# Kernel tuning notes

Measured on AMD Instinct MI355X. Metric: run time of the kernel, lower is better.

Reference implementation:

```python
import jax, jax.numpy as jnp
import numpy as np

WS = 8          # window_size
NH = 8          # num_heads
DIM = 512
INNER = 512
CDIM = 128
CINNER = 128
SHIFTED = True
EPS = 1e-6
N = WS * WS     # tokens per window
SCALE = 1.0 / np.sqrt(INNER // NH + CINNER // NH)  # SDPA scale over fused (feat+coord) head dim


def _rmsnorm(x, g):
    return x * jax.lax.rsqrt(jnp.mean(x * x, axis=-1, keepdims=True) + EPS) * g


def _rel_indices():
    idx = np.array([[x, y] for x in range(WS) for y in range(WS)])
    ri = idx[None, :, :] - idx[:, None, :] + WS - 1
    return ri[..., 0], ri[..., 1]


def _shift_mask(Wh, Ww):
    s = WS
    k = s * (s // 2)
    row = np.zeros((N, N), np.float32)
    row[-k:, :-k] = -np.inf
    row[:-k, -k:] = -np.inf
    col = row.reshape(s, s, s, s).transpose(1, 0, 3, 2).reshape(N, N)
    m = np.zeros((Wh, Ww, N, N), np.float32)
    m[:, -1] += row
    m[-1, :] += col
    return jnp.asarray(m)


def setup_inputs() -> dict:
    key = jax.random.key(0)
    ks = jax.random.split(key, 16)
    B, h, w = 4, 128, 128

    def lin(k, fan_in, fan_out):
        return jax.random.normal(k, (fan_in, fan_out), jnp.float32) * (fan_in ** -0.5)

    return {
        "features": jax.random.normal(ks[0], (B, h, w, DIM), jnp.float32),
        "coords": jax.random.normal(ks[1], (B, h, w, CDIM), jnp.float32),
        "w_fqk": lin(ks[2], DIM, 2 * INNER),
        "b_fqk": jnp.zeros((2 * INNER,), jnp.float32),
        "g_fqk": jnp.ones((2 * INNER,), jnp.float32),
        "w_cqk": lin(ks[3], CDIM, 2 * CINNER),
        "b_cqk": jnp.zeros((2 * CINNER,), jnp.float32),
        "g_cqk": jnp.ones((2 * CINNER,), jnp.float32),
        "w_v": lin(ks[4], DIM, INNER),
        "b_v": jnp.zeros((INNER,), jnp.float32),
        "w_out": lin(ks[5], INNER, DIM),
        "b_out": jnp.zeros((DIM,), jnp.float32),
        "pos_emb": jax.random.normal(ks[6], (2 * WS - 1, 2 * WS - 1), jnp.float32),
    }


def reference(features, coords, w_fqk, b_fqk, g_fqk, w_cqk, b_cqk, g_cqk,
              w_v, b_v, w_out, b_out, pos_emb):
    B, h, w, _ = features.shape
    pad_h = (WS - h % WS) % WS
    pad_w = (WS - w % WS) % WS
    H_pad, W_pad = h + pad_h, w + pad_w
    Wh, Ww = H_pad // WS, W_pad // WS

    fqk = _rmsnorm(features @ w_fqk + b_fqk, g_fqk)
    f_q, f_k = jnp.split(fqk, 2, axis=-1)
    cqk = _rmsnorm(coords @ w_cqk + b_cqk, g_cqk)
    c_q, c_k = jnp.split(cqk, 2, axis=-1)
    f_v = features @ w_v + b_v

    def win(t):
        t = jnp.pad(t, ((0, 0), (0, pad_h), (0, pad_w), (0, 0)))
        if SHIFTED:
            t = jnp.roll(t, (-(WS // 2), -(WS // 2)), axis=(1, 2))
        D = t.shape[-1]
        t = t.reshape(B, Wh, WS, Ww, WS, D).transpose(0, 1, 3, 2, 4, 5)
        return t.reshape(B, Wh, Ww, N, D)

    def heads(t):
        D = t.shape[-1]
        return t.reshape(B, Wh, Ww, N, NH, D // NH)

    fq, fk, fv = heads(win(f_q)), heads(win(f_k)), heads(win(f_v))
    cq, ck = heads(win(c_q)), heads(win(c_k))

    # fused feature + coordinate QK scores, per head per window
    scores = (jnp.einsum('bxyqhd,bxykhd->bxyhqk', fq, fk)
              + jnp.einsum('bxyqhd,bxykhd->bxyhqk', cq, ck)) * SCALE

    ri0, ri1 = _rel_indices()
    pos_bias = pos_emb[ri0, ri1]  # (N, N)
    bias = pos_bias[None, None, None, None]
    if SHIFTED:
        bias = bias + _shift_mask(Wh, Ww)[None, :, :, None]
    scores = scores + bias

    attn = jax.nn.softmax(scores, axis=-1)
    out = jnp.einsum('bxyhqk,bxykhd->bxyqhd', attn, fv)
    out = out.reshape(B, Wh, Ww, N, INNER)

    # un-window
    out = out.reshape(B, Wh, Ww, WS, WS, INNER).transpose(0, 1, 3, 2, 4, 5)
    out = out.reshape(B, H_pad, W_pad, INNER)
    if SHIFTED:
        out = jnp.roll(out, (WS // 2, WS // 2), axis=(1, 2))
    out = out[:, :h, :w, :]
    return out @ w_out + b_out
```

## Files before the change

### kernel.cpp

```cpp
#include <hip/hip_runtime.h>
#include <hip/hip_bf16.h>
#include <type_traits>

using bf16 = __hip_bfloat16;
typedef __bf16 bf16x8 __attribute__((ext_vector_type(8)));
typedef float f32x4 __attribute__((ext_vector_type(4)));

static constexpr int TOKENS = 4 * 128 * 128;
#define SCALE_F 0.11180339887498949f
#define EPS_F 1e-6f

__device__ __forceinline__ float u2f(unsigned short u) {
  union { unsigned int i; float f; } c; c.i = (unsigned int)u << 16; return c.f;
}
__device__ __forceinline__ unsigned short f2u(float f) {
  bf16 h = __float2bfloat16(f); return *reinterpret_cast<unsigned short*>(&h);
}
__device__ __forceinline__ float b2f(bf16 v) { return __bfloat162float(v); }
__device__ __forceinline__ int4 cvt8(const float* p) {
  float4 a = ((const float4*)p)[0], b = ((const float4*)p)[1];
  union { int4 i4; unsigned short s[8]; } u;
  u.s[0] = f2u(a.x); u.s[1] = f2u(a.y); u.s[2] = f2u(a.z); u.s[3] = f2u(a.w);
  u.s[4] = f2u(b.x); u.s[5] = f2u(b.y); u.s[6] = f2u(b.z); u.s[7] = f2u(b.w);
  return u.i4;
}
__device__ __forceinline__ void gload16(const bf16* g, bf16* l) {
  __builtin_amdgcn_global_load_lds(
      (const __attribute__((address_space(1))) unsigned int*)g,
      (__attribute__((address_space(3))) unsigned int*)l, 16, 0, 0);
}

__global__ void convert_k(const float* __restrict__ in, bf16* __restrict__ out,
                          long n) {
  long i = ((long)blockIdx.x * 256 + threadIdx.x) * 8;
  long stride = (long)gridDim.x * 256 * 8;
  for (; i < n; i += stride) *(int4*)(out + i) = cvt8(in + i);
}

__global__ void transpose_k(const float* __restrict__ in, bf16* __restrict__ out,
                            int K, int N) {
  int i = blockIdx.x * 256 + threadIdx.x;
  if (i >= K * N) return;
  int k = i / N, n = i - k * N;
  out[(size_t)n * K + k] = __float2bfloat16(in[i]);
}

__global__ void biascat_k(const float* __restrict__ a, const float* __restrict__ b,
                          float* __restrict__ o) {
  int i = blockIdx.x * 256 + threadIdx.x;
  if (i < 1536) o[i] = i < 1024 ? a[i] : b[i - 1024];
}

template <typename TC, int SSNX>
__global__ __launch_bounds__(256) void gemm128_k(
    const bf16* __restrict__ A, const bf16* __restrict__ Wt,
    const float* __restrict__ bias, TC* __restrict__ C,
    float* __restrict__ ssq, int M, int N, int K) {
  __shared__ __align__(16) bf16 sA[2][4096];
  __shared__ __align__(16) bf16 sB[2][4096];
  const int t = threadIdx.x, lane = t & 63, wave = t >> 6;
  const int wr = wave >> 1, wc = wave & 1;
  const int nwg = gridDim.x * gridDim.y;
  int id = blockIdx.y * gridDim.x + blockIdx.x;
  if ((nwg & 7) == 0) id = (id & 7) * (nwg >> 3) + (id >> 3);
  const int bx = id % gridDim.x, by = id / gridDim.x;
  const int bm = by * 128, bn = bx * 128;
  const int l15 = lane & 15, kg = lane >> 4;
  f32x4 acc[4][4] = {};

  const int srow = t >> 2;
  const int ske = ((t & 3) ^ ((srow >> 1) & 3)) * 8;
  const bf16* pA0 = A + (size_t)(bm + srow) * K + ske;
  const bf16* pA1 = A + (size_t)(bm + 64 + srow) * K + ske;
  const bf16* pB0 = Wt + (size_t)(bn + srow) * K + ske;
  const bf16* pB1 = Wt + (size_t)(bn + 64 + srow) * K + ske;
  const int wo = wave * 512;

  gload16(pA0, &sA[0][wo]);
  gload16(pA1, &sA[0][2048 + wo]);
  gload16(pB0, &sB[0][wo]);
  gload16(pB1, &sB[0][2048 + wo]);
  __syncthreads();

  const int nt = K >> 5;
  int cur = 0;
  for (int tt = 0; tt < nt; ++tt) {
    if (tt + 1 < nt) {
      pA0 += 32; pA1 += 32; pB0 += 32; pB1 += 32;
      gload16(pA0, &sA[cur ^ 1][wo]);
      gload16(pA1, &sA[cur ^ 1][2048 + wo]);
      gload16(pB0, &sB[cur ^ 1][wo]);
      gload16(pB1, &sB[cur ^ 1][2048 + wo]);
    }
    bf16x8 wf[4], xf[4];
#pragma unroll
    for (int i = 0; i < 4; ++i) {
      int frow = wc * 64 + i * 16 + l15;
      int xrow = wr * 64 + i * 16 + l15;
      wf[i] = *(const bf16x8*)(&sB[cur][frow * 32 + ((kg ^ ((frow >> 1) & 3)) * 8)]);
      xf[i] = *(const bf16x8*)(&sA[cur][xrow * 32 + ((kg ^ ((xrow >> 1) & 3)) * 8)]);
    }
#pragma unroll
    for (int i = 0; i < 4; ++i)
#pragma unroll
      for (int j = 0; j < 4; ++j)
        acc[i][j] = __builtin_amdgcn_mfma_f32_16x16x32_bf16(wf[i], xf[j], acc[i][j], 0, 0, 0);
    __syncthreads();
    cur ^= 1;
  }

  float bvi[4][4];
#pragma unroll
  for (int i = 0; i < 4; ++i) {
    float4 b4 = *(const float4*)(bias + bn + wc * 64 + i * 16 + kg * 4);
    bvi[i][0] = b4.x; bvi[i][1] = b4.y; bvi[i][2] = b4.z; bvi[i][3] = b4.w;
  }
#pragma unroll
  for (int j = 0; j < 4; ++j) {
    const int token = bm + wr * 64 + j * 16 + l15;
    float ssum = 0.f;
#pragma unroll
    for (int i = 0; i < 4; ++i) {
      float v0 = acc[i][j][0] + bvi[i][0];
      float v1 = acc[i][j][1] + bvi[i][1];
      float v2 = acc[i][j][2] + bvi[i][2];
      float v3 = acc[i][j][3] + bvi[i][3];
      const size_t off = (size_t)token * N + bn + wc * 64 + i * 16 + kg * 4;
      if constexpr (std::is_same<TC, float>::value) {
        *(float4*)(C + off) = float4{v0, v1, v2, v3};
      } else {
        ushort4 pk{f2u(v0), f2u(v1), f2u(v2), f2u(v3)};
        *(ushort4*)(C + off) = pk;
      }
      if constexpr (SSNX > 0)
        ssum += v0 * v0 + v1 * v1 + v2 * v2 + v3 * v3;
    }
    if constexpr (SSNX > 0) {
      ssum += __shfl_xor(ssum, 16);
      ssum += __shfl_xor(ssum, 32);
      if (bx < SSNX && kg == 0)
        ssq[(size_t)token * (SSNX * 2) + bx * 2 + wc] = ssum;
    }
  }
}

__global__ void finalize_rs_k(const float* __restrict__ pf,
                              const float* __restrict__ pc,
                              float* __restrict__ rsf, float* __restrict__ rsc) {
  int i = blockIdx.x * 256 + threadIdx.x;
  if (i >= TOKENS) return;
  float s = 0.f;
#pragma unroll
  for (int j = 0; j < 16; ++j) s += pf[(size_t)i * 16 + j];
  rsf[i] = rsqrtf(s * (1.f / 1024.f) + EPS_F);
  float c = 0.f;
#pragma unroll
  for (int j = 0; j < 4; ++j) c += pc[(size_t)i * 4 + j];
  rsc[i] = rsqrtf(c * (1.f / 256.f) + EPS_F);
}

__global__ __launch_bounds__(256) void attn_mfma_k(
    const bf16* __restrict__ qkv, const bf16* __restrict__ cqk,
    const float* __restrict__ pos, const float* __restrict__ g_fqk,
    const float* __restrict__ g_cqk, const float* __restrict__ rs_f,
    const float* __restrict__ rs_c, bf16* __restrict__ aout) {
  __shared__ __align__(16) bf16 sQ[64][104], sK[64][104];
  __shared__ __align__(16) bf16 sVt[64][72];
  __shared__ __align__(16) bf16 sP[64][72];
  __shared__ float sPos[15][15];
  __shared__ float sRsF[64], sRsC[64];
  const int t = threadIdx.x, lane = t & 63, wave = t >> 6;
  const int head = blockIdx.x & 7;
  const int wid = blockIdx.x >> 3;
  const int wx = wid & 15, wy = (wid >> 4) & 15, b = wid >> 8;

  for (int i = t; i < 225; i += 256) sPos[i / 15][i % 15] = pos[i];
  if (t < 64) {
    const int y = ((wy << 3) + (t >> 3) + 4) & 127;
    const int x = ((wx << 3) + (t & 7) + 4) & 127;
    const size_t tok = ((size_t)b << 14) | (y << 7) | x;
    sRsF[t] = rs_f[tok];
    sRsC[t] = rs_c[tok];
  }
  {
    const int n = t >> 2, p = t & 3;
    const int y = ((wy << 3) + (n >> 3) + 4) & 127;
    const int x = ((wx << 3) + (n & 7) + 4) & 127;
    const size_t tok = ((size_t)b << 14) | (y << 7) | x;
    const bf16* row = qkv + tok * 1536;
    const int4* qp = (const int4*)(row + head * 64 + p * 16);
    ((int4*)&sQ[n][p * 16])[0] = qp[0];
    ((int4*)&sQ[n][p * 16])[1] = qp[1];
    {
      const bf16* kpp = row + 512 + head * 64 + p * 16;
      const float* gq = g_fqk + head * 64 + p * 16;
      const float* gk = g_fqk + 512 + head * 64 + p * 16;
      union { int4 v[2]; unsigned short s[16]; } kt;
#pragma unroll
      for (int i = 0; i < 16; ++i)
        kt.s[i] = f2u(b2f(kpp[i]) * gq[i] * gk[i]);
      ((int4*)&sK[n][p * 16])[0] = kt.v[0];
      ((int4*)&sK[n][p * 16])[1] = kt.v[1];
    }
    const bf16* vp = row + 1024 + head * 64 + p * 16;
#pragma unroll
    for (int i = 0; i < 16; ++i) sVt[p * 16 + i][n] = vp[i];
    const bf16* crow = cqk + tok * 256;
    if (p == 0) {
      const int4* cp = (const int4*)(crow + head * 16);
      ((int4*)&sQ[n][64])[0] = cp[0];
      ((int4*)&sQ[n][64])[1] = cp[1];
    } else if (p == 1) {
      const bf16* ckp = crow + 128 + head * 16;
      const float* gcq = g_cqk + head * 16;
      const float* gck = g_cqk + 128 + head * 16;
      union { int4 v[2]; unsigned short s[16]; } ct;
#pragma unroll
      for (int i = 0; i < 16; ++i)
        ct.s[i] = f2u(b2f(ckp[i]) * gcq[i] * gck[i]);
      ((int4*)&sK[n][64])[0] = ct.v[0];
      ((int4*)&sK[n][64])[1] = ct.v[1];
    } else if (p == 2) {
      ((int4*)&sQ[n][80])[0] = int4{0, 0, 0, 0};
      ((int4*)&sQ[n][80])[1] = int4{0, 0, 0, 0};
    } else {
      ((int4*)&sK[n][80])[0] = int4{0, 0, 0, 0};
      ((int4*)&sK[n][80])[1] = int4{0, 0, 0, 0};
    }
  }
  __syncthreads();

  const int l15 = lane & 15, kg = lane >> 4;
  bf16x8 qa[3];
#pragma unroll
  for (int ko = 0; ko < 3; ++ko)
    qa[ko] = *(const bf16x8*)&sQ[wave * 16 + l15][ko * 32 + kg * 8];
  f32x4 saccf[4] = {}, saccc[4] = {};
#pragma unroll
  for (int j = 0; j < 4; ++j) {
#pragma unroll
    for (int ko = 0; ko < 2; ++ko) {
      bf16x8 kb = *(const bf16x8*)&sK[j * 16 + l15][ko * 32 + kg * 8];
      saccf[j] = __builtin_amdgcn_mfma_f32_16x16x32_bf16(qa[ko], kb, saccf[j], 0, 0, 0);
    }
    bf16x8 kb2 = *(const bf16x8*)&sK[j * 16 + l15][64 + kg * 8];
    saccc[j] = __builtin_amdgcn_mfma_f32_16x16x32_bf16(qa[2], kb2, saccc[j], 0, 0, 0);
  }

  const bool lastx = (wx == 15), lasty = (wy == 15);
  float rqf[4], rqc[4];
#pragma unroll
  for (int r = 0; r < 4; ++r) {
    rqf[r] = sRsF[wave * 16 + kg * 4 + r];
    rqc[r] = sRsC[wave * 16 + kg * 4 + r];
  }
  float sv[4][4], mx[4], sum[4], inv[4];
#pragma unroll
  for (int r = 0; r < 4; ++r) mx[r] = -1e30f;
#pragma unroll
  for (int j = 0; j < 4; ++j) {
    int kcol = j * 16 + l15, kh = kcol >> 3, kw = kcol & 7;
    float rkf = sRsF[kcol], rkc = sRsC[kcol];
#pragma unroll
    for (int r = 0; r < 4; ++r) {
      int q = wave * 16 + kg * 4 + r, qh = q >> 3, qw = q & 7;
      bool msk = (lastx && ((qh >= 4) != (kh >= 4))) ||
                 (lasty && ((qw >= 4) != (kw >= 4)));
      float raw = saccf[j][r] * rqf[r] * rkf + saccc[j][r] * rqc[r] * rkc;
      float val = msk ? -1e30f : raw * SCALE_F + sPos[kh - qh + 7][kw - qw + 7];
      sv[j][r] = val;
      mx[r] = fmaxf(mx[r], val);
    }
  }
#pragma unroll
  for (int m = 1; m < 16; m <<= 1)
#pragma unroll
    for (int r = 0; r < 4; ++r) mx[r] = fmaxf(mx[r], __shfl_xor(mx[r], m));
#pragma unroll
  for (int r = 0; r < 4; ++r) sum[r] = 0.f;
#pragma unroll
  for (int j = 0; j < 4; ++j) {
    int kcol = j * 16 + l15;
#pragma unroll
    for (int r = 0; r < 4; ++r) {
      float e = __expf(sv[j][r] - mx[r]);
      sum[r] += e;
      sP[wave * 16 + kg * 4 + r][kcol] = __float2bfloat16(e);
    }
  }
#pragma unroll
  for (int m = 1; m < 16; m <<= 1)
#pragma unroll
    for (int r = 0; r < 4; ++r) sum[r] += __shfl_xor(sum[r], m);
#pragma unroll
  for (int r = 0; r < 4; ++r) inv[r] = 1.f / sum[r];
  __syncthreads();

  bf16x8 pa[2];
#pragma unroll
  for (int ko = 0; ko < 2; ++ko)
    pa[ko] = *(const bf16x8*)&sP[wave * 16 + l15][ko * 32 + kg * 8];
  f32x4 oacc[4] = {};
#pragma unroll
  for (int jf = 0; jf < 4; ++jf)
#pragma unroll
    for (int ko = 0; ko < 2; ++ko) {
      bf16x8 vb = *(const bf16x8*)&sVt[jf * 16 + l15][ko * 32 + kg * 8];
      oacc[jf] = __builtin_amdgcn_mfma_f32_16x16x32_bf16(pa[ko], vb, oacc[jf], 0, 0, 0);
    }
#pragma unroll
  for (int r = 0; r < 4; ++r) {
    int q = wave * 16 + kg * 4 + r;
    const int y = ((wy << 3) + (q >> 3) + 4) & 127;
    const int x = ((wx << 3) + (q & 7) + 4) & 127;
    const size_t tok = ((size_t)b << 14) | (y << 7) | x;
    bf16* dst = aout + tok * 512 + head * 64;
#pragma unroll
    for (int jf = 0; jf < 4; ++jf)
      dst[jf * 16 + l15] = __float2bfloat16(oacc[jf][r] * inv[r]);
  }
}

extern "C" void kernel_launch(void* const* d_in, const int* in_sizes, int n_in,
                              void* d_out, int out_size, void* d_ws, size_t ws_size,
                              hipStream_t stream) {
  const float* features = (const float*)d_in[0];
  const float* coords   = (const float*)d_in[1];
  const float* w_fqk = (const float*)d_in[2];
  const float* b_fqk = (const float*)d_in[3];
  const float* g_fqk = (const float*)d_in[4];
  const float* w_cqk = (const float*)d_in[5];
  const float* b_cqk = (const float*)d_in[6];
  const float* g_cqk = (const float*)d_in[7];
  const float* w_v   = (const float*)d_in[8];
  const float* b_v   = (const float*)d_in[9];
  const float* w_out = (const float*)d_in[10];
  const float* b_out = (const float*)d_in[11];
  const float* pos_emb = (const float*)d_in[12];
  float* out = (float*)d_out;

  const int M = TOKENS;
  bf16* qkv   = (bf16*)d_ws;
  bf16* cqk   = qkv + (size_t)M * 1536;
  bf16* aout  = cqk + (size_t)M * 256;
  bf16* wcombT = aout + (size_t)M * 512;
  bf16* wcqkT  = wcombT + (size_t)1536 * 512;
  bf16* woutT  = wcqkT + 256 * 128;
  float* bias_comb = (float*)(woutT + 512 * 512);
  float* ssq_f = bias_comb + 1536;
  float* ssq_c = ssq_f + (size_t)M * 16;
  float* rs_f  = ssq_c + (size_t)M * 4;
  float* rs_c  = rs_f + M;
  bf16* fb16 = (bf16*)d_out;
  bf16* cb16 = fb16 + (size_t)M * 512;

  convert_k<<<2048, 256, 0, stream>>>(features, fb16, (long)M * 512);
  convert_k<<<1024, 256, 0, stream>>>(coords, cb16, (long)M * 128);
  transpose_k<<<(512 * 1024 + 255) / 256, 256, 0, stream>>>(w_fqk, wcombT, 512, 1024);
  transpose_k<<<(512 * 512 + 255) / 256, 256, 0, stream>>>(w_v, wcombT + (size_t)1024 * 512, 512, 512);
  transpose_k<<<(128 * 256 + 255) / 256, 256, 0, stream>>>(w_cqk, wcqkT, 128, 256);
  transpose_k<<<(512 * 512 + 255) / 256, 256, 0, stream>>>(w_out, woutT, 512, 512);
  biascat_k<<<6, 256, 0, stream>>>(b_fqk, b_v, bias_comb);

  gemm128_k<bf16, 8><<<dim3(12, 512), 256, 0, stream>>>(fb16, wcombT, bias_comb, qkv, ssq_f, M, 1536, 512);
  gemm128_k<bf16, 2><<<dim3(2, 512), 256, 0, stream>>>(cb16, wcqkT, b_cqk, cqk, ssq_c, M, 256, 128);
  finalize_rs_k<<<TOKENS / 256, 256, 0, stream>>>(ssq_f, ssq_c, rs_f, rs_c);
  attn_mfma_k<<<4 * 16 * 16 * 8, 256, 0, stream>>>(qkv, cqk, pos_emb, g_fqk, g_cqk, rs_f, rs_c, aout);
  gemm128_k<float, 0><<<dim3(4, 512), 256, 0, stream>>>(aout, woutT, b_out, out, nullptr, M, 512, 512);
}
```

Measured before the change: 417.2 us.

## Replace 128x128 GEMMs with 256x256 triple-buffered 8-wave GEMM kernel

```diff
diff --git a/kernel.cpp b/kernel.cpp
--- a/kernel.cpp
+++ b/kernel.cpp
@@ -49,6 +49,119 @@
                           float* __restrict__ o) {
   int i = blockIdx.x * 256 + threadIdx.x;
   if (i < 1536) o[i] = i < 1024 ? a[i] : b[i - 1024];
+}
+
+template <int QF>
+__device__ __forceinline__ void mfma16(f32x4 (&acc)[8][4], const bf16x8 (&wfr)[4],
+                                       const bf16x8 (&xfr)[4]) {
+#pragma unroll
+  for (int fi = 0; fi < 4; ++fi)
+#pragma unroll
+    for (int j = 0; j < 4; ++j)
+      acc[QF * 4 + fi][j] =
+          __builtin_amdgcn_mfma_f32_16x16x32_bf16(wfr[fi], xfr[j], acc[QF * 4 + fi][j], 0, 0, 0);
+}
+
+template <typename TC, int SSNX>
+__global__ __launch_bounds__(512, 2) void gemm256_k(
+    const bf16* __restrict__ A, const bf16* __restrict__ Wt,
+    const float* __restrict__ bias, TC* __restrict__ C,
+    float* __restrict__ ssq, int M, int N, int K) {
+  extern __shared__ __align__(16) bf16 smem[];
+  bf16* sX = smem;
+  bf16* sW = smem + 24576;
+  const int t = threadIdx.x, lane = t & 63, wave = t >> 6;
+  const int wm = wave >> 2, wn = wave & 3;
+  const int l15 = lane & 15, kg = lane >> 4;
+  const int nwg = gridDim.x * gridDim.y;
+  int id = blockIdx.y * gridDim.x + blockIdx.x;
+  id = (id & 7) * (nwg >> 3) + (id >> 3);
+  const int bx = id % gridDim.x, by = id / gridDim.x;
+  const int bm = by * 256, bn = bx * 256;
+  f32x4 acc[8][4] = {};
+
+  const int srow = t >> 2;
+  const int sw8 = ((t & 3) ^ ((srow >> 1) & 3)) * 8;
+  const int sdst = srow * 32 + (t & 3) * 8;
+  const int fsw = (kg ^ ((l15 >> 1) & 3)) * 8;
+
+  auto stageX = [&](int buf, int k0) {
+    bf16* d = sX + buf * 8192 + sdst;
+    gload16(A + (size_t)(bm + srow) * K + k0 + sw8, d);
+    gload16(A + (size_t)(bm + 128 + srow) * K + k0 + sw8, d + 4096);
+  };
+  auto stageW = [&](int buf, int k0) {
+    bf16* d = sW + buf * 8192 + sdst;
+    gload16(Wt + (size_t)(bn + srow) * K + k0 + sw8, d);
+    gload16(Wt + (size_t)(bn + 128 + srow) * K + k0 + sw8, d + 4096);
+  };
+
+  const int NT = K >> 5;
+  stageX(0, 0); stageW(0, 0); stageX(1, 32); stageW(1, 32);
+
+  int buf = 0;
+  for (int u = 0; u < NT; ++u) {
+    if (u < NT - 1) asm volatile("s_waitcnt vmcnt(4)" ::: "memory");
+    else            asm volatile("s_waitcnt vmcnt(0)" ::: "memory");
+    __builtin_amdgcn_s_barrier();
+    __builtin_amdgcn_sched_barrier(0);
+    int nb = buf + 2; if (nb >= 3) nb -= 3;
+    if (u + 2 < NT) stageX(nb, (u + 2) * 32);
+    bf16x8 xfr[4], wfr[4];
+    const bf16* bX = sX + buf * 8192;
+    const bf16* bW = sW + buf * 8192;
+#pragma unroll
+    for (int j = 0; j < 4; ++j)
+      xfr[j] = *(const bf16x8*)(bX + (wn * 64 + j * 16 + l15) * 32 + fsw);
+#pragma unroll
+    for (int fi = 0; fi < 4; ++fi)
+      wfr[fi] = *(const bf16x8*)(bW + (wm * 128 + fi * 16 + l15) * 32 + fsw);
+    __builtin_amdgcn_s_setprio(1);
+    mfma16<0>(acc, wfr, xfr);
+    __builtin_amdgcn_s_setprio(0);
+    if (u + 2 < NT) stageW(nb, (u + 2) * 32);
+#pragma unroll
+    for (int fi = 0; fi < 4; ++fi)
+      wfr[fi] = *(const bf16x8*)(bW + (wm * 128 + 64 + fi * 16 + l15) * 32 + fsw);
+    __builtin_amdgcn_s_setprio(1);
+    mfma16<1>(acc, wfr, xfr);
+    __builtin_amdgcn_s_setprio(0);
+    buf = (buf == 2) ? 0 : buf + 1;
+  }
+
+  float bvi[8][4];
+#pragma unroll
+  for (int i = 0; i < 8; ++i) {
+    float4 b4 = *(const float4*)(bias + bn + wm * 128 + (i >> 2) * 64 + (i & 3) * 16 + kg * 4);
+    bvi[i][0] = b4.x; bvi[i][1] = b4.y; bvi[i][2] = b4.z; bvi[i][3] = b4.w;
+  }
+#pragma unroll
+  for (int j = 0; j < 4; ++j) {
+    const int token = bm + wn * 64 + j * 16 + l15;
+    float ssum = 0.f;
+#pragma unroll
+    for (int i = 0; i < 8; ++i) {
+      float v0 = acc[i][j][0] + bvi[i][0];
+      float v1 = acc[i][j][1] + bvi[i][1];
+      float v2 = acc[i][j][2] + bvi[i][2];
+      float v3 = acc[i][j][3] + bvi[i][3];
+      const size_t off = (size_t)token * N + bn + wm * 128 + (i >> 2) * 64 + (i & 3) * 16 + kg * 4;
+      if constexpr (std::is_same<TC, float>::value) {
+        *(float4*)(C + off) = float4{v0, v1, v2, v3};
+      } else {
+        ushort4 pk{f2u(v0), f2u(v1), f2u(v2), f2u(v3)};
+        *(ushort4*)(C + off) = pk;
+      }
+      if constexpr (SSNX > 0)
+        ssum += v0 * v0 + v1 * v1 + v2 * v2 + v3 * v3;
+    }
+    if constexpr (SSNX > 0) {
+      ssum += __shfl_xor(ssum, 16);
+      ssum += __shfl_xor(ssum, 32);
+      if (bx < SSNX && kg == 0)
+        ssq[(size_t)token * (SSNX * 2) + bx * 2 + wm] = ssum;
+    }
+  }
 }
 
 template <typename TC, int SSNX>
@@ -151,7 +264,7 @@
   if (i >= TOKENS) return;
   float s = 0.f;
 #pragma unroll
-  for (int j = 0; j < 16; ++j) s += pf[(size_t)i * 16 + j];
+  for (int j = 0; j < 8; ++j) s += pf[(size_t)i * 8 + j];
   rsf[i] = rsqrtf(s * (1.f / 1024.f) + EPS_F);
   float c = 0.f;
 #pragma unroll
@@ -348,7 +461,7 @@
   bf16* woutT  = wcqkT + 256 * 128;
   float* bias_comb = (float*)(woutT + 512 * 512);
   float* ssq_f = bias_comb + 1536;
-  float* ssq_c = ssq_f + (size_t)M * 16;
+  float* ssq_c = ssq_f + (size_t)M * 8;
   float* rs_f  = ssq_c + (size_t)M * 4;
   float* rs_c  = rs_f + M;
   bf16* fb16 = (bf16*)d_out;
@@ -362,9 +475,9 @@
   transpose_k<<<(512 * 512 + 255) / 256, 256, 0, stream>>>(w_out, woutT, 512, 512);
   biascat_k<<<6, 256, 0, stream>>>(b_fqk, b_v, bias_comb);
 
-  gemm128_k<bf16, 8><<<dim3(12, 512), 256, 0, stream>>>(fb16, wcombT, bias_comb, qkv, ssq_f, M, 1536, 512);
+  gemm256_k<bf16, 4><<<dim3(6, 256), 512, 98304, stream>>>(fb16, wcombT, bias_comb, qkv, ssq_f, M, 1536, 512);
   gemm128_k<bf16, 2><<<dim3(2, 512), 256, 0, stream>>>(cb16, wcqkT, b_cqk, cqk, ssq_c, M, 256, 128);
   finalize_rs_k<<<TOKENS / 256, 256, 0, stream>>>(ssq_f, ssq_c, rs_f, rs_c);
   attn_mfma_k<<<4 * 16 * 16 * 8, 256, 0, stream>>>(qkv, cqk, pos_emb, g_fqk, g_cqk, rs_f, rs_c, aout);
-  gemm128_k<float, 0><<<dim3(4, 512), 256, 0, stream>>>(aout, woutT, b_out, out, nullptr, M, 512, 512);
-}
+  gemm256_k<float, 0><<<dim3(2, 256), 512, 98304, stream>>>(aout, woutT, b_out, out, nullptr, M, 512, 512);
+}
```

Measured after the change: 385.0 us. 1.08x faster.

## Add 256x128-tile 512-thread GEMM for QKV and output projections; reorder attention grid

Applied to the files above, without the earlier changes.

```diff
diff --git a/kernel.cpp b/kernel.cpp
--- a/kernel.cpp
+++ b/kernel.cpp
@@ -49,6 +49,95 @@
                           float* __restrict__ o) {
   int i = blockIdx.x * 256 + threadIdx.x;
   if (i < 1536) o[i] = i < 1024 ? a[i] : b[i - 1024];
+}
+
+template <typename TC, int SSNX>
+__global__ __launch_bounds__(512, 4) void gemm256h_k(
+    const bf16* __restrict__ A, const bf16* __restrict__ Wt,
+    const float* __restrict__ bias, TC* __restrict__ C,
+    float* __restrict__ ssq, int M, int N, int K) {
+  __shared__ __align__(16) bf16 sX[2][8192];
+  __shared__ __align__(16) bf16 sW[2][4096];
+  const int t = threadIdx.x, lane = t & 63, wave = t >> 6;
+  const int wm = wave >> 2, wn = wave & 3;
+  const int l15 = lane & 15, kg = lane >> 4;
+  const int nwg = gridDim.x * gridDim.y;
+  int id = blockIdx.y * gridDim.x + blockIdx.x;
+  id = (id & 7) * (nwg >> 3) + (id >> 3);
+  const int bx = id % gridDim.x, by = id / gridDim.x;
+  const int bm = by * 256, bn = bx * 128;
+  f32x4 acc[4][4] = {};
+
+  const int srow = t >> 2;
+  const int ske = ((t & 3) ^ ((srow >> 1) & 3)) * 8;
+  auto stX = [&](int buf, int k0) {
+    gload16(A + (size_t)(bm + srow) * K + k0 + ske, &sX[buf][t * 8]);
+    gload16(A + (size_t)(bm + 128 + srow) * K + k0 + ske, &sX[buf][4096 + t * 8]);
+  };
+  auto stW = [&](int buf, int k0) {
+    gload16(Wt + (size_t)(bn + srow) * K + k0 + ske, &sW[buf][t * 8]);
+  };
+
+  stX(0, 0); stW(0, 0);
+  __syncthreads();
+
+  const int NT = K >> 5;
+  int cur = 0;
+  for (int g = 0; g < NT; ++g) {
+    if (g + 1 < NT) { stX(cur ^ 1, (g + 1) << 5); stW(cur ^ 1, (g + 1) << 5); }
+    bf16x8 wf[4], xf[4];
+#pragma unroll
+    for (int i = 0; i < 4; ++i) {
+      int frow = wm * 64 + i * 16 + l15;
+      wf[i] = *(const bf16x8*)(&sW[cur][frow * 32 + ((kg ^ ((frow >> 1) & 3)) * 8)]);
+    }
+#pragma unroll
+    for (int j = 0; j < 4; ++j) {
+      int xrow = wn * 64 + j * 16 + l15;
+      xf[j] = *(const bf16x8*)(&sX[cur][xrow * 32 + ((kg ^ ((xrow >> 1) & 3)) * 8)]);
+    }
+#pragma unroll
+    for (int i = 0; i < 4; ++i)
+#pragma unroll
+      for (int j = 0; j < 4; ++j)
+        acc[i][j] = __builtin_amdgcn_mfma_f32_16x16x32_bf16(wf[i], xf[j], acc[i][j], 0, 0, 0);
+    __syncthreads();
+    cur ^= 1;
+  }
+
+  float bvi[4][4];
+#pragma unroll
+  for (int i = 0; i < 4; ++i) {
+    float4 b4 = *(const float4*)(bias + bn + wm * 64 + i * 16 + kg * 4);
+    bvi[i][0] = b4.x; bvi[i][1] = b4.y; bvi[i][2] = b4.z; bvi[i][3] = b4.w;
+  }
+#pragma unroll
+  for (int j = 0; j < 4; ++j) {
+    const int token = bm + wn * 64 + j * 16 + l15;
+    float ssum = 0.f;
+#pragma unroll
+    for (int i = 0; i < 4; ++i) {
+      float v0 = acc[i][j][0] + bvi[i][0];
+      float v1 = acc[i][j][1] + bvi[i][1];
+      float v2 = acc[i][j][2] + bvi[i][2];
+      float v3 = acc[i][j][3] + bvi[i][3];
+      const size_t off = (size_t)token * N + bn + wm * 64 + i * 16 + kg * 4;
+      if constexpr (std::is_same<TC, float>::value) {
+        *(float4*)(C + off) = float4{v0, v1, v2, v3};
+      } else {
+        ushort4 pk{f2u(v0), f2u(v1), f2u(v2), f2u(v3)};
+        *(ushort4*)(C + off) = pk;
+      }
+      if constexpr (SSNX > 0)
+        ssum += v0 * v0 + v1 * v1 + v2 * v2 + v3 * v3;
+    }
+    if constexpr (SSNX > 0) {
+      ssum += __shfl_xor(ssum, 16);
+      ssum += __shfl_xor(ssum, 32);
+      if (bx < SSNX && kg == 0)
+        ssq[(size_t)token * (SSNX * 2) + bx * 2 + wm] = ssum;
+    }
+  }
 }
 
 template <typename TC, int SSNX>
@@ -170,8 +259,8 @@
   __shared__ float sPos[15][15];
   __shared__ float sRsF[64], sRsC[64];
   const int t = threadIdx.x, lane = t & 63, wave = t >> 6;
-  const int head = blockIdx.x & 7;
-  const int wid = blockIdx.x >> 3;
+  const int head = blockIdx.x >> 10;
+  const int wid = blockIdx.x & 1023;
   const int wx = wid & 15, wy = (wid >> 4) & 15, b = wid >> 8;
 
   for (int i = t; i < 225; i += 256) sPos[i / 15][i % 15] = pos[i];
@@ -362,9 +451,9 @@
   transpose_k<<<(512 * 512 + 255) / 256, 256, 0, stream>>>(w_out, woutT, 512, 512);
   biascat_k<<<6, 256, 0, stream>>>(b_fqk, b_v, bias_comb);
 
-  gemm128_k<bf16, 8><<<dim3(12, 512), 256, 0, stream>>>(fb16, wcombT, bias_comb, qkv, ssq_f, M, 1536, 512);
+  gemm256h_k<bf16, 8><<<dim3(12, 256), 512, 0, stream>>>(fb16, wcombT, bias_comb, qkv, ssq_f, M, 1536, 512);
   gemm128_k<bf16, 2><<<dim3(2, 512), 256, 0, stream>>>(cb16, wcqkT, b_cqk, cqk, ssq_c, M, 256, 128);
   finalize_rs_k<<<TOKENS / 256, 256, 0, stream>>>(ssq_f, ssq_c, rs_f, rs_c);
-  attn_mfma_k<<<4 * 16 * 16 * 8, 256, 0, stream>>>(qkv, cqk, pos_emb, g_fqk, g_cqk, rs_f, rs_c, aout);
-  gemm128_k<float, 0><<<dim3(4, 512), 256, 0, stream>>>(aout, woutT, b_out, out, nullptr, M, 512, 512);
-}
+  attn_mfma_k<<<8 * 1024, 256, 0, stream>>>(qkv, cqk, pos_emb, g_fqk, g_cqk, rs_f, rs_c, aout);
+  gemm256h_k<float, 0><<<dim3(4, 256), 512, 0, stream>>>(aout, woutT, b_out, out, nullptr, M, 512, 512);
+}
```

New measurement: 395.5 us. 5.2% less time.
